# Performance work log

Hardware: AMD Instinct MI355X
Metric: run time of the kernel (lower is better)

Reference implementation:

```python
import jax, jax.numpy as jnp
import numpy as np

S, I, H, C, B = 512, 1, 256, 10, 2048

def _xavier(key, shape):
    fan_out, fan_in = shape
    std = (2.0 / (fan_in + fan_out)) ** 0.5
    return jax.random.normal(key, shape, dtype=jnp.float32) * std

def setup_inputs() -> dict:
    key = jax.random.key(0)
    k_x, k_hx, k_hh, k_ph = jax.random.split(key, 4)
    return {
        "x": jax.random.normal(k_x, (B, S), dtype=jnp.float32),
        "W_hx": _xavier(k_hx, (H, I)),
        "W_hh": _xavier(k_hh, (H, H)),
        "W_ph": _xavier(k_ph, (C, H)),
        "b_h": jnp.zeros((H, 1), dtype=jnp.float32),
        "b_p": jnp.zeros((C, 1), dtype=jnp.float32),
    }

def reference(x, W_hx, W_hh, W_ph, b_h, b_p):
    # x: [B, S]; hidden state h: [H, B]
    batch = x.shape[0]
    h0 = jnp.zeros((W_hh.shape[0], batch), dtype=x.dtype)
    xs = x.T  # [S, B], one row per timestep

    def step(h, x_t):
        # x_t: [B] -> [1, B]; W_hx: [H, 1]
        h_new = jnp.tanh(W_hx @ x_t[None, :] + W_hh @ h + b_h)
        return h_new, None

    h_final, _ = jax.lax.scan(step, h0, xs)
    # output: [B, C]
    return (W_ph @ h_final + b_p).T
```

## Files before the change

kernel.cpp:

```cpp
#include <hip/hip_runtime.h>


#define SEQ   512
#define HID   256
#define NCLS  10
#define BN    16
#define NT    512

typedef _Float16 f16x8 __attribute__((ext_vector_type(8)));
typedef _Float16 f16x4 __attribute__((ext_vector_type(4)));
typedef float    f32x4 __attribute__((ext_vector_type(4)));

__global__ __launch_bounds__(NT)
__attribute__((amdgpu_waves_per_eu(2, 2)))
void rnn_mfma(
    const float* __restrict__ x,
    const float* __restrict__ W_hx,
    const float* __restrict__ W_hh,
    const float* __restrict__ W_ph,
    const float* __restrict__ b_h,
    const float* __restrict__ b_p,
    float* __restrict__ out)
{
    __shared__ __align__(16) _Float16 hT[2][BN][HID];
    __shared__ __align__(16) float xs[SEQ + 2][BN];

    const int tid  = threadIdx.x;
    const int lane = tid & 63;
    const int wave = tid >> 6;
    const int n16  = lane & 15;
    const int quad = lane >> 4;
    const int e    = n16 & 7;
    const int b0   = blockIdx.x * BN;

    const float SC = 2.885390081777926814f;

    f16x8 afrag[2][8];
#pragma unroll
    for (int mt = 0; mt < 2; ++mt) {
        const int row = wave * 32 + mt * 16 + n16;
#pragma unroll
        for (int ks = 0; ks < 8; ++ks) {
            const float4* p = (const float4*)&W_hh[row * HID + ks * 32 + quad * 8];
            float4 u = p[0], v = p[1];
            f16x8 a;
            a[0] = (_Float16)(SC * u.x); a[1] = (_Float16)(SC * u.y);
            a[2] = (_Float16)(SC * u.z); a[3] = (_Float16)(SC * u.w);
            a[4] = (_Float16)(SC * v.x); a[5] = (_Float16)(SC * v.y);
            a[6] = (_Float16)(SC * v.z); a[7] = (_Float16)(SC * v.w);
            afrag[mt][ks] = a;
        }
    }
    f32x4 bias[2], wxv[2];
#pragma unroll
    for (int mt = 0; mt < 2; ++mt)
#pragma unroll
        for (int r = 0; r < 4; ++r) {
            const int row = wave * 32 + mt * 16 + quad * 4 + r;
            bias[mt][r] = SC * b_h[row];
            wxv[mt][r]  = SC * W_hx[row];
        }

    int roff[8], woff[2];
#pragma unroll
    for (int ks = 0; ks < 8; ++ks)
        roff[ks] = (n16 * HID + (((4 * ks + quad) ^ e) << 3)) * 2;
#pragma unroll
    for (int mt = 0; mt < 2; ++mt)
        woff[mt] = (n16 * HID +
                    (((4 * wave + 2 * mt + (quad >> 1)) ^ e) << 3) +
                    (quad & 1) * 4) * 2;

    for (int i = tid; i < BN * SEQ / 4; i += NT) {
        const int n = i >> 7, t4 = (i & 127) * 4;
        float4 v = *(const float4*)&x[(b0 + n) * SEQ + t4];
        xs[t4 + 0][n] = v.x; xs[t4 + 1][n] = v.y;
        xs[t4 + 2][n] = v.z; xs[t4 + 3][n] = v.w;
    }
    for (int i = tid; i < BN * HID / 2; i += NT) ((float*)hT[0])[i] = 0.0f;
    __syncthreads();

    float xv = xs[0][n16];

#define RNN_STEP(T, RD, WR)                                                   \
    {                                                                         \
        const float xnxt = xs[(T) + 1][n16];      \
        const char* hb = (const char*)hT[RD];                                 \
        f16x8 bfr[8];                                                         \
        _Pragma("unroll")                                                     \
        for (int ks = 0; ks < 8; ++ks)                                        \
            bfr[ks] = *(const f16x8*)(hb + roff[ks]);                         \
        f32x4 acc[2];                                                         \
        _Pragma("unroll")                                                     \
        for (int mt = 0; mt < 2; ++mt) {                                      \
            f32x4 c0;                                                         \
            _Pragma("unroll")                                                 \
            for (int r = 0; r < 4; ++r)                                       \
                c0[r] = fmaf(wxv[mt][r], xv, bias[mt][r]);                    \
            acc[mt] = __builtin_amdgcn_mfma_f32_16x16x32_f16(                 \
                afrag[mt][0], bfr[0], c0, 0, 0, 0);                           \
        }                                                                     \
        _Pragma("unroll")                                                     \
        for (int ks = 1; ks < 8; ++ks)                                        \
            _Pragma("unroll")                                                 \
            for (int mt = 0; mt < 2; ++mt)                                    \
                acc[mt] = __builtin_amdgcn_mfma_f32_16x16x32_f16(             \
                    afrag[mt][ks], bfr[ks], acc[mt], 0, 0, 0);                \
        char* wb = (char*)hT[WR];                                             \
        _Pragma("unroll")                                                     \
        for (int mt = 0; mt < 2; ++mt) {                                      \
            f16x4 h4;                                                         \
            _Pragma("unroll")                                                 \
            for (int r = 0; r < 4; ++r) {                                     \
                float ex = __builtin_amdgcn_exp2f(acc[mt][r]);                \
                float rc = __builtin_amdgcn_rcpf(ex + 1.0f);                  \
                h4[r] = (_Float16)(1.0f - 2.0f * rc);                         \
            }                                                                 \
            *(f16x4*)(wb + woff[mt]) = h4;                                    \
        }                                                                     \
        xv = xnxt;                                                            \
        __syncthreads();                                                      \
    }

    for (int t = 0; t < SEQ; t += 2) {
        RNN_STEP(t, 0, 1);
        RNN_STEP(t + 1, 1, 0);
    }
#undef RNN_STEP

    if (tid < BN * NCLS) {
        const int b = tid / NCLS, c = tid % NCLS;
        float sum = b_p[c];
        const _Float16* hp = hT[0][b];
        for (int j = 0; j < HID; ++j) {
            const int ph = ((((j >> 3) ^ (b & 7)) << 3) | (j & 7));
            sum += W_ph[c * HID + j] * (float)hp[ph];
        }
        out[(b0 + b) * NCLS + c] = sum;
    }
}

extern "C" void kernel_launch(void* const* d_in, const int* in_sizes, int n_in,
                              void* d_out, int out_size, void* d_ws, size_t ws_size,
                              hipStream_t stream) {
    const float* x    = (const float*)d_in[0];
    const float* W_hx = (const float*)d_in[1];
    const float* W_hh = (const float*)d_in[2];
    const float* W_ph = (const float*)d_in[3];
    const float* b_h  = (const float*)d_in[4];
    const float* b_p  = (const float*)d_in[5];
    float* out = (float*)d_out;

    rnn_mfma<<<dim3(2048 / BN), dim3(NT), 0, stream>>>(
        x, W_hx, W_hh, W_ph, b_h, b_p, out);
}
```

Before: 330.5 us.

## Halve batch tile to 8 and split MFMA accumulation into two chains

Cuts the per-block batch tile from 16 to 8, which doubles the grid to 256 blocks so more CUs are used, at the cost of wasting half of each 16-wide MFMA N dimension. Lanes 8-15 duplicate columns 0-7 and skip the writeback. The K reduction is split into two independent accumulator chains so consecutive MFMAs do not wait on each other, which shortens the serial dependency per step. The x staging buffer uses a padded pitch of 9 to avoid bank conflicts.

```diff
diff --git a/kernel.cpp b/kernel.cpp
--- a/kernel.cpp
+++ b/kernel.cpp
@@ -1,11 +1,12 @@
 #include <hip/hip_runtime.h>
 
 
-#define SEQ   512
-#define HID   256
-#define NCLS  10
-#define BN    16
-#define NT    512
+#define SEQ    512
+#define HID    256
+#define NCLS   10
+#define BN     8
+#define NT     512
+#define XPITCH 9
 
 typedef _Float16 f16x8 __attribute__((ext_vector_type(8)));
 typedef _Float16 f16x4 __attribute__((ext_vector_type(4)));
@@ -23,14 +24,14 @@
     float* __restrict__ out)
 {
     __shared__ __align__(16) _Float16 hT[2][BN][HID];
-    __shared__ __align__(16) float xs[SEQ + 2][BN];
+    __shared__ __align__(16) float xs[SEQ + 2][XPITCH];
 
     const int tid  = threadIdx.x;
     const int lane = tid & 63;
     const int wave = tid >> 6;
     const int n16  = lane & 15;
     const int quad = lane >> 4;
-    const int e    = n16 & 7;
+    const int nb   = n16 & 7;
     const int b0   = blockIdx.x * BN;
 
     const float SC = 2.885390081777926814f;
@@ -64,11 +65,11 @@
     int roff[8], woff[2];
 #pragma unroll
     for (int ks = 0; ks < 8; ++ks)
-        roff[ks] = (n16 * HID + (((4 * ks + quad) ^ e) << 3)) * 2;
+        roff[ks] = (nb * HID + (((4 * ks + quad) ^ nb) << 3)) * 2;
 #pragma unroll
     for (int mt = 0; mt < 2; ++mt)
-        woff[mt] = (n16 * HID +
-                    (((4 * wave + 2 * mt + (quad >> 1)) ^ e) << 3) +
+        woff[mt] = (nb * HID +
+                    (((4 * wave + 2 * mt + (quad >> 1)) ^ nb) << 3) +
                     (quad & 1) * 4) * 2;
 
     for (int i = tid; i < BN * SEQ / 4; i += NT) {
@@ -80,43 +81,51 @@
     for (int i = tid; i < BN * HID / 2; i += NT) ((float*)hT[0])[i] = 0.0f;
     __syncthreads();
 
-    float xv = xs[0][n16];
+    float xv = xs[0][nb];
 
 #define RNN_STEP(T, RD, WR)                                                   \
     {                                                                         \
-        const float xnxt = xs[(T) + 1][n16];      \
+        const float xnxt = xs[(T) + 1][nb];       \
         const char* hb = (const char*)hT[RD];                                 \
         f16x8 bfr[8];                                                         \
         _Pragma("unroll")                                                     \
         for (int ks = 0; ks < 8; ++ks)                                        \
             bfr[ks] = *(const f16x8*)(hb + roff[ks]);                         \
-        f32x4 acc[2];                                                         \
+        f32x4 acc0[2], acc1[2];                                               \
         _Pragma("unroll")                                                     \
         for (int mt = 0; mt < 2; ++mt) {                                      \
             f32x4 c0;                                                         \
             _Pragma("unroll")                                                 \
             for (int r = 0; r < 4; ++r)                                       \
                 c0[r] = fmaf(wxv[mt][r], xv, bias[mt][r]);                    \
-            acc[mt] = __builtin_amdgcn_mfma_f32_16x16x32_f16(                 \
+            acc0[mt] = __builtin_amdgcn_mfma_f32_16x16x32_f16(                \
                 afrag[mt][0], bfr[0], c0, 0, 0, 0);                           \
+            acc1[mt] = __builtin_amdgcn_mfma_f32_16x16x32_f16(                \
+                afrag[mt][1], bfr[1], (f32x4)0.0f, 0, 0, 0);                  \
         }                                                                     \
         _Pragma("unroll")                                                     \
-        for (int ks = 1; ks < 8; ++ks)                                        \
+        for (int ks = 2; ks < 8; ks += 2)                                     \
             _Pragma("unroll")                                                 \
-            for (int mt = 0; mt < 2; ++mt)                                    \
-                acc[mt] = __builtin_amdgcn_mfma_f32_16x16x32_f16(             \
-                    afrag[mt][ks], bfr[ks], acc[mt], 0, 0, 0);                \
+            for (int mt = 0; mt < 2; ++mt) {                                  \
+                acc0[mt] = __builtin_amdgcn_mfma_f32_16x16x32_f16(            \
+                    afrag[mt][ks], bfr[ks], acc0[mt], 0, 0, 0);               \
+                acc1[mt] = __builtin_amdgcn_mfma_f32_16x16x32_f16(            \
+                    afrag[mt][ks + 1], bfr[ks + 1], acc1[mt], 0, 0, 0);       \
+            }                                                                 \
         char* wb = (char*)hT[WR];                                             \
+        f16x4 h4[2];                                                          \
         _Pragma("unroll")                                                     \
-        for (int mt = 0; mt < 2; ++mt) {                                      \
-            f16x4 h4;                                                         \
+        for (int mt = 0; mt < 2; ++mt)                                        \
             _Pragma("unroll")                                                 \
             for (int r = 0; r < 4; ++r) {                                     \
-                float ex = __builtin_amdgcn_exp2f(acc[mt][r]);                \
+                float s  = acc0[mt][r] + acc1[mt][r];                         \
+                float ex = __builtin_amdgcn_exp2f(s);                         \
                 float rc = __builtin_amdgcn_rcpf(ex + 1.0f);                  \
-                h4[r] = (_Float16)(1.0f - 2.0f * rc);                         \
+                h4[mt][r] = (_Float16)(1.0f - 2.0f * rc);                     \
             }                                                                 \
-            *(f16x4*)(wb + woff[mt]) = h4;                                    \
+        if (n16 < 8) {                                                        \
+            *(f16x4*)(wb + woff[0]) = h4[0];                                  \
+            *(f16x4*)(wb + woff[1]) = h4[1];                                  \
         }                                                                     \
         xv = xnxt;                                                            \
         __syncthreads();                                                      \
@@ -133,7 +142,7 @@
         float sum = b_p[c];
         const _Float16* hp = hT[0][b];
         for (int j = 0; j < HID; ++j) {
-            const int ph = ((((j >> 3) ^ (b & 7)) << 3) | (j & 7));
+            const int ph = ((((j >> 3) ^ b) << 3) | (j & 7));
             sum += W_ph[c * HID + j] * (float)hp[ph];
         }
         out[(b0 + b) * NCLS + c] = sum;
```

Result: slower. 340.7 us (+3.1%).

## Replace XOR swizzle with padded LDS pitch and stagger per-wave k-order

Applied to the files above, without the earlier changes.

Drops the XOR-swizzled hidden-state layout and uses a padded row pitch of 264 halves, plus a padded x staging buffer. Waves 4-7 walk the k-slices in a rotated order so the two halves of the block read different LDS banks at the same moment. The B-fragment loads are split into two groups of four, with the second group issued between MFMAs, to overlap LDS latency with compute and cut register pressure. The bigger risk is the padded layout, which may bring back bank conflicts that the swizzle was avoiding.

```diff
diff --git a/kernel.cpp b/kernel.cpp
--- a/kernel.cpp
+++ b/kernel.cpp
@@ -1,15 +1,19 @@
 #include <hip/hip_runtime.h>
 
 
-#define SEQ   512
-#define HID   256
-#define NCLS  10
-#define BN    16
-#define NT    512
+#define SEQ    512
+#define HID    256
+#define NCLS   10
+#define BN     16
+#define NT     512
+#define XP     17
+#define PITCH  264
 
 typedef _Float16 f16x8 __attribute__((ext_vector_type(8)));
 typedef _Float16 f16x4 __attribute__((ext_vector_type(4)));
 typedef float    f32x4 __attribute__((ext_vector_type(4)));
+
+#define MFMA16(a, b, c) __builtin_amdgcn_mfma_f32_16x16x32_f16(a, b, c, 0, 0, 0)
 
 __global__ __launch_bounds__(NT)
 __attribute__((amdgpu_waves_per_eu(2, 2)))
@@ -22,15 +26,14 @@
     const float* __restrict__ b_p,
     float* __restrict__ out)
 {
-    __shared__ __align__(16) _Float16 hT[2][BN][HID];
-    __shared__ __align__(16) float xs[SEQ + 2][BN];
+    __shared__ __align__(16) _Float16 hT[2][BN][PITCH];
+    __shared__ __align__(16) float xs[SEQ + 2][XP];
 
     const int tid  = threadIdx.x;
     const int lane = tid & 63;
     const int wave = tid >> 6;
     const int n16  = lane & 15;
     const int quad = lane >> 4;
-    const int e    = n16 & 7;
     const int b0   = blockIdx.x * BN;
 
     const float SC = 2.885390081777926814f;
@@ -61,15 +64,8 @@
             wxv[mt][r]  = SC * W_hx[row];
         }
 
-    int roff[8], woff[2];
-#pragma unroll
-    for (int ks = 0; ks < 8; ++ks)
-        roff[ks] = (n16 * HID + (((4 * ks + quad) ^ e) << 3)) * 2;
-#pragma unroll
-    for (int mt = 0; mt < 2; ++mt)
-        woff[mt] = (n16 * HID +
-                    (((4 * wave + 2 * mt + (quad >> 1)) ^ e) << 3) +
-                    (quad & 1) * 4) * 2;
+    const int rbase = n16 * (PITCH * 2) + quad * 16;
+    const int wbase = n16 * (PITCH * 2) + wave * 64 + quad * 8;
 
     for (int i = tid; i < BN * SEQ / 4; i += NT) {
         const int n = i >> 7, t4 = (i & 127) * 4;
@@ -77,19 +73,21 @@
         xs[t4 + 0][n] = v.x; xs[t4 + 1][n] = v.y;
         xs[t4 + 2][n] = v.z; xs[t4 + 3][n] = v.w;
     }
-    for (int i = tid; i < BN * HID / 2; i += NT) ((float*)hT[0])[i] = 0.0f;
+    for (int i = tid; i < BN * PITCH / 2; i += NT) ((float*)hT[0])[i] = 0.0f;
     __syncthreads();
 
     float xv = xs[0][n16];
 
-#define RNN_STEP(T, RD, WR)                                                   \
+#define RNN_STEP(T, RD, WR, P)                                                \
     {                                                                         \
         const float xnxt = xs[(T) + 1][n16];      \
-        const char* hb = (const char*)hT[RD];                                 \
-        f16x8 bfr[8];                                                         \
-        _Pragma("unroll")                                                     \
-        for (int ks = 0; ks < 8; ++ks)                                        \
-            bfr[ks] = *(const f16x8*)(hb + roff[ks]);                         \
+        const char* rb = (const char*)hT[RD] + rbase;                         \
+        char*       wb = (char*)hT[WR] + wbase;                               \
+                                                \
+        f16x8 bA0 = *(const f16x8*)(rb + (((P) + 0) & 7) * 64);               \
+        f16x8 bA1 = *(const f16x8*)(rb + (((P) + 1) & 7) * 64);               \
+        f16x8 bA2 = *(const f16x8*)(rb + (((P) + 2) & 7) * 64);               \
+        f16x8 bA3 = *(const f16x8*)(rb + (((P) + 3) & 7) * 64);               \
         f32x4 acc[2];                                                         \
         _Pragma("unroll")                                                     \
         for (int mt = 0; mt < 2; ++mt) {                                      \
@@ -97,16 +95,27 @@
             _Pragma("unroll")                                                 \
             for (int r = 0; r < 4; ++r)                                       \
                 c0[r] = fmaf(wxv[mt][r], xv, bias[mt][r]);                    \
-            acc[mt] = __builtin_amdgcn_mfma_f32_16x16x32_f16(                 \
-                afrag[mt][0], bfr[0], c0, 0, 0, 0);                           \
+            acc[mt] = MFMA16(afrag[mt][((P) + 0) & 7], bA0, c0);              \
         }                                                                     \
-        _Pragma("unroll")                                                     \
-        for (int ks = 1; ks < 8; ++ks)                                        \
-            _Pragma("unroll")                                                 \
-            for (int mt = 0; mt < 2; ++mt)                                    \
-                acc[mt] = __builtin_amdgcn_mfma_f32_16x16x32_f16(             \
-                    afrag[mt][ks], bfr[ks], acc[mt], 0, 0, 0);                \
-        char* wb = (char*)hT[WR];                                             \
+        acc[0] = MFMA16(afrag[0][((P) + 1) & 7], bA1, acc[0]);                \
+        acc[1] = MFMA16(afrag[1][((P) + 1) & 7], bA1, acc[1]);                \
+                                      \
+        f16x8 bB0 = *(const f16x8*)(rb + (((P) + 4) & 7) * 64);               \
+        f16x8 bB1 = *(const f16x8*)(rb + (((P) + 5) & 7) * 64);               \
+        f16x8 bB2 = *(const f16x8*)(rb + (((P) + 6) & 7) * 64);               \
+        f16x8 bB3 = *(const f16x8*)(rb + (((P) + 7) & 7) * 64);               \
+        acc[0] = MFMA16(afrag[0][((P) + 2) & 7], bA2, acc[0]);                \
+        acc[1] = MFMA16(afrag[1][((P) + 2) & 7], bA2, acc[1]);                \
+        acc[0] = MFMA16(afrag[0][((P) + 3) & 7], bA3, acc[0]);                \
+        acc[1] = MFMA16(afrag[1][((P) + 3) & 7], bA3, acc[1]);                \
+        acc[0] = MFMA16(afrag[0][((P) + 4) & 7], bB0, acc[0]);                \
+        acc[1] = MFMA16(afrag[1][((P) + 4) & 7], bB0, acc[1]);                \
+        acc[0] = MFMA16(afrag[0][((P) + 5) & 7], bB1, acc[0]);                \
+        acc[1] = MFMA16(afrag[1][((P) + 5) & 7], bB1, acc[1]);                \
+        acc[0] = MFMA16(afrag[0][((P) + 6) & 7], bB2, acc[0]);                \
+        acc[1] = MFMA16(afrag[1][((P) + 6) & 7], bB2, acc[1]);                \
+        acc[0] = MFMA16(afrag[0][((P) + 7) & 7], bB3, acc[0]);                \
+        acc[1] = MFMA16(afrag[1][((P) + 7) & 7], bB3, acc[1]);                \
         _Pragma("unroll")                                                     \
         for (int mt = 0; mt < 2; ++mt) {                                      \
             f16x4 h4;                                                         \
@@ -116,15 +125,22 @@
                 float rc = __builtin_amdgcn_rcpf(ex + 1.0f);                  \
                 h4[r] = (_Float16)(1.0f - 2.0f * rc);                         \
             }                                                                 \
-            *(f16x4*)(wb + woff[mt]) = h4;                                    \
+            *(f16x4*)(wb + mt * 32) = h4;                                     \
         }                                                                     \
         xv = xnxt;                                                            \
         __syncthreads();                                                      \
     }
 
-    for (int t = 0; t < SEQ; t += 2) {
-        RNN_STEP(t, 0, 1);
-        RNN_STEP(t + 1, 1, 0);
+    if (((wave >> 2) & 1) == 0) {
+        for (int t = 0; t < SEQ; t += 2) {
+            RNN_STEP(t,     0, 1, 0)
+            RNN_STEP(t + 1, 1, 0, 0)
+        }
+    } else {
+        for (int t = 0; t < SEQ; t += 2) {
+            RNN_STEP(t,     0, 1, 4)
+            RNN_STEP(t + 1, 1, 0, 4)
+        }
     }
 #undef RNN_STEP
 
@@ -132,10 +148,8 @@
         const int b = tid / NCLS, c = tid % NCLS;
         float sum = b_p[c];
         const _Float16* hp = hT[0][b];
-        for (int j = 0; j < HID; ++j) {
-            const int ph = ((((j >> 3) ^ (b & 7)) << 3) | (j & 7));
-            sum += W_ph[c * HID + j] * (float)hp[ph];
-        }
+        for (int j = 0; j < HID; ++j)
+            sum += W_ph[c * HID + j] * (float)hp[j];
         out[(b0 + b) * NCLS + c] = sum;
     }
 }
```

Result: no change. 332.4 us (+0.6%).
